# Performance work log

Hardware: AMD Instinct MI355X
Metric: run time of the kernel (lower is better)

The kernel has to match this reference:

```python
import jax, jax.numpy as jnp
import numpy as np

EMB = 64          # emb_size
LG = 64           # lg_msg_dim
NDB = 16          # num_dist_basis
NCB = 16          # num_cos_basis
NCLS = 40
NLAYERS = 2
NJK = NLAYERS + 2  # jumping-knowledge sequence length
HID = (NJK * EMB) // 2  # PyG JK-LSTM hidden size = 128


def setup_inputs() -> dict:
    key = jax.random.key(0)
    ks = jax.random.split(key, 24)
    N, Eg, Elg, F = 50000, 800000, 800000, 128
    s = 0.05
    inp = {
        "x": jax.random.normal(ks[0], (N, F), jnp.float32),
        "edge_index_g": jax.random.randint(ks[1], (2, Eg), 0, N, jnp.int32),
        "edge_attr_g": jax.random.uniform(ks[2], (Eg, NDB), jnp.float32),
        "edge_index_lg": jax.random.randint(ks[3], (2, Elg), 0, Eg, jnp.int32),
        "edge_attr_lg": jax.random.uniform(ks[4], (Elg, NCB), jnp.float32),
        # parameters (nn.Linear convention: W is [out, in])
        "W_feat": jax.random.normal(ks[5], (EMB, F), jnp.float32) * s,
        "W_msg": jax.random.normal(ks[6], (LG, 2 * EMB + NDB), jnp.float32) * s,
        "W_lg2g": jax.random.normal(ks[7], (EMB, LG), jnp.float32) * s,
        "b_lg2g": jax.random.normal(ks[8], (EMB,), jnp.float32) * s,
        "W_msg_layers": jax.random.normal(ks[9], (NLAYERS, LG, 2 * LG + NCB), jnp.float32) * s,
        # bidirectional LSTM params (PyTorch gate order i,f,g,o)
        "Wih_f": jax.random.normal(ks[10], (4 * HID, EMB), jnp.float32) * s,
        "Whh_f": jax.random.normal(ks[11], (4 * HID, HID), jnp.float32) * s,
        "bih_f": jax.random.normal(ks[12], (4 * HID,), jnp.float32) * s,
        "bhh_f": jax.random.normal(ks[13], (4 * HID,), jnp.float32) * s,
        "Wih_b": jax.random.normal(ks[14], (4 * HID, EMB), jnp.float32) * s,
        "Whh_b": jax.random.normal(ks[15], (4 * HID, HID), jnp.float32) * s,
        "bih_b": jax.random.normal(ks[16], (4 * HID,), jnp.float32) * s,
        "bhh_b": jax.random.normal(ks[17], (4 * HID,), jnp.float32) * s,
        "W_att": jax.random.normal(ks[18], (1, 2 * HID), jnp.float32) * s,
        "b_att": jax.random.normal(ks[19], (1,), jnp.float32) * s,
        "W_out": jax.random.normal(ks[20], (NCLS, EMB), jnp.float32) * s,
    }
    return inp


def _lstm(x_seq, Wih, Whh, bih, bhh, reverse):
    # x_seq: [N, L, C] -> hs: [N, L, H]
    N = x_seq.shape[0]
    H = Whh.shape[1]
    b = bih + bhh

    def step(carry, x_t):
        h, c = carry
        gates = x_t @ Wih.T + h @ Whh.T + b
        i, f, g, o = jnp.split(gates, 4, axis=-1)
        c = jax.nn.sigmoid(f) * c + jax.nn.sigmoid(i) * jnp.tanh(g)
        h = jax.nn.sigmoid(o) * jnp.tanh(c)
        return (h, c), h

    xs = jnp.swapaxes(x_seq, 0, 1)  # [L, N, C]
    init = (jnp.zeros((N, H), x_seq.dtype), jnp.zeros((N, H), x_seq.dtype))
    _, hs = jax.lax.scan(step, init, xs, reverse=reverse)
    return jnp.swapaxes(hs, 0, 1)


def reference(x, edge_index_g, edge_attr_g, edge_index_lg, edge_attr_lg,
              W_feat, W_msg, W_lg2g, b_lg2g, W_msg_layers,
              Wih_f, Whh_f, bih_f, bhh_f, Wih_b, Whh_b, bih_b, bhh_b,
              W_att, b_att, W_out):
    N = x.shape[0]
    Eg = edge_attr_g.shape[0]
    seg = jax.ops.segment_sum

    # node embedding (eval mode: dropout is identity)
    node_emb = jax.nn.relu(x @ W_feat.T)  # [N, EMB]

    # initial linegraph node features: gather endpoints -> concat -> linear -> relu
    m1 = node_emb[edge_index_g[0]]  # [Eg, EMB]
    m2 = node_emb[edge_index_g[1]]
    msg_emb = jax.nn.relu(jnp.concatenate([m1, m2, edge_attr_g], -1) @ W_msg.T)  # [Eg, LG]

    node_embs = [node_emb]
    msg_red = msg_emb @ W_lg2g.T + b_lg2g
    node_embs.append(seg(msg_red, edge_index_g[1], num_segments=N))

    # message-passing layers on the linegraph
    for l in range(W_msg_layers.shape[0]):
        s = msg_emb[edge_index_lg[0]]
        d = msg_emb[edge_index_lg[1]]
        m = jax.nn.relu(jnp.concatenate([s, d, edge_attr_lg], -1) @ W_msg_layers[l].T)
        msg_emb = seg(m, edge_index_lg[1], num_segments=Eg)  # scatter_add over linegraph
        incoming = seg(msg_emb, edge_index_g[1], num_segments=N)
        node_embs.append(incoming @ W_lg2g.T + b_lg2g)

    # JumpingKnowledge ('lstm'): bidirectional LSTM -> attention -> weighted sum
    x_jk = jnp.stack(node_embs, axis=1)  # [N, NJK, EMB]
    h_f = _lstm(x_jk, Wih_f, Whh_f, bih_f, bhh_f, reverse=False)
    h_b = _lstm(x_jk, Wih_b, Whh_b, bih_b, bhh_b, reverse=True)
    h = jnp.concatenate([h_f, h_b], -1)  # [N, NJK, 2*HID]
    alpha = jax.nn.softmax((h @ W_att.T + b_att)[..., 0], axis=-1)  # [N, NJK]
    final_emb = jnp.sum(x_jk * alpha[..., None], axis=1)  # [N, EMB]

    out = final_emb @ W_out.T
    return jax.nn.log_softmax(out, axis=-1)
```

## Files before the change

### kernel.cpp

```cpp
#include <hip/hip_runtime.h>

typedef unsigned short u16;
typedef unsigned int u32;
typedef __attribute__((ext_vector_type(8))) short bf16x8;
typedef __attribute__((ext_vector_type(4))) float f32x4;

#define MFMA(a, b, c) __builtin_amdgcn_mfma_f32_16x16x32_bf16(a, b, c, 0, 0, 0)

__device__ __forceinline__ u16 f2bf(float x) {
    union { float f; u32 u; } v; v.f = x;
    u32 r = (v.u + 0x7FFFu + ((v.u >> 16) & 1u)) >> 16;
    return (u16)r;
}
__device__ __forceinline__ float bf2f(u16 b) {
    union { u32 u; float f; } v; v.u = ((u32)b) << 16;
    return v.f;
}
__device__ __forceinline__ void casAddPair(u32* w, float lo, float hi) {
    u32 old = *w, assumed;
    do {
        assumed = old;
        u32 des = (u32)f2bf(bf2f((u16)(assumed & 0xFFFFu)) + lo) |
                  ((u32)f2bf(bf2f((u16)(assumed >> 16)) + hi) << 16);
        if (des == assumed) break;
        old = atomicCAS(w, assumed, des);
    } while (old != assumed);
}

__global__ __launch_bounds__(256) void prep_w(
    const float* __restrict__ Whh_f, const float* __restrict__ Whh_b,
    const float* __restrict__ Wih_f, const float* __restrict__ Wih_b,
    const float* __restrict__ bih_f, const float* __restrict__ bhh_f,
    const float* __restrict__ bih_b, const float* __restrict__ bhh_b,
    const float* __restrict__ W_feat, const float* __restrict__ W_msg,
    const float* __restrict__ W_msg_l, const float* __restrict__ W_lg2g,
    u16* __restrict__ WhhB, u16* __restrict__ WihB, float* __restrict__ BS,
    u16* __restrict__ WfeatB, u16* __restrict__ WmsgB,
    u16* __restrict__ WmsgLB, u16* __restrict__ Wlg2gB)
{
    const float L2E = 1.4426950408889634f;
    int i = blockIdx.x * 256 + threadIdx.x;
    if (i < 131072) {
        int d = i >> 16, r = i & 65535;
        float s = (((r >> 14) & 3) == 2) ? 2.f * L2E : L2E;
        WhhB[i] = f2bf(s * (d ? Whh_b[r] : Whh_f[r]));
    } else if (i < 196608) {
        int i2 = i - 131072; int d = i2 >> 15, r = i2 & 32767;
        float s = (((r >> 13) & 3) == 2) ? 2.f * L2E : L2E;
        WihB[i2] = f2bf(s * (d ? Wih_b[r] : Wih_f[r]));
    } else if (i < 197632) {
        int i3 = i - 196608; int d = i3 >> 9, g = i3 & 511;
        float s = (((g >> 7) & 3) == 2) ? 2.f * L2E : L2E;
        BS[i3] = s * (d ? (bih_b[g] + bhh_b[g]) : (bih_f[g] + bhh_f[g]));
    } else if (i < 205824) {
        int j = i - 197632; WfeatB[j] = f2bf(W_feat[j]);
    } else if (i < 215040) {
        int j = i - 205824; WmsgB[j] = f2bf(W_msg[j]);
    } else if (i < 233472) {
        int j = i - 215040; WmsgLB[j] = f2bf(W_msg_l[j]);
    } else if (i < 237568) {
        int j = i - 233472; Wlg2gB[j] = f2bf(W_lg2g[j]);
    }
}

__global__ __launch_bounds__(256) void count_kernel(const int* __restrict__ dst,
                                                    u32* __restrict__ cnt, long E)
{
    long i = (long)blockIdx.x * 256 + threadIdx.x;
    if (i < E) atomicAdd(&cnt[dst[i]], 1u);
}

__global__ __launch_bounds__(256) void scan1(const u32* __restrict__ a,
                                             u32* __restrict__ part, int n)
{
    __shared__ u32 ts[256];
    int b = blockIdx.x, t = threadIdx.x;
    long i0 = (long)b * 1024 + t * 4;
    u32 s = 0;
#pragma unroll
    for (int k = 0; k < 4; ++k) { long i = i0 + k; if (i < n) s += a[i]; }
    ts[t] = s; __syncthreads();
    for (int off = 1; off < 256; off <<= 1) {
        u32 x = (t >= off) ? ts[t - off] : 0u;
        __syncthreads(); ts[t] += x; __syncthreads();
    }
    if (t == 255) part[b] = ts[255];
}

__global__ __launch_bounds__(1024) void scan2(u32* __restrict__ part, int nb,
                                              u32* __restrict__ total_out)
{
    __shared__ u32 ts[1024];
    int t = threadIdx.x;
    u32 v = (t < nb) ? part[t] : 0u;
    ts[t] = v; __syncthreads();
    for (int off = 1; off < 1024; off <<= 1) {
        u32 x = (t >= off) ? ts[t - off] : 0u;
        __syncthreads(); ts[t] += x; __syncthreads();
    }
    if (t < nb) part[t] = ts[t] - v;
    if (t == 1023 && total_out) *total_out = ts[1023];
}

__global__ __launch_bounds__(256) void scan3(u32* __restrict__ a,
                                             const u32* __restrict__ part, int n)
{
    __shared__ u32 ts[256];
    int b = blockIdx.x, t = threadIdx.x;
    long i0 = (long)b * 1024 + t * 4;
    u32 v[4]; u32 s = 0;
#pragma unroll
    for (int k = 0; k < 4; ++k) { long i = i0 + k; v[k] = (i < n) ? a[i] : 0u; s += v[k]; }
    ts[t] = s; __syncthreads();
    for (int off = 1; off < 256; off <<= 1) {
        u32 x = (t >= off) ? ts[t - off] : 0u;
        __syncthreads(); ts[t] += x; __syncthreads();
    }
    u32 run = part[b] + ts[t] - s;
#pragma unroll
    for (int k = 0; k < 4; ++k) {
        long i = i0 + k;
        if (i < n) { u32 x = v[k]; a[i] = run; run += x; }
    }
}

__global__ __launch_bounds__(256) void fill_kernel(const int* __restrict__ dst,
                                                   u32* __restrict__ off,
                                                   int* __restrict__ list, long E)
{
    long i = (long)blockIdx.x * 256 + threadIdx.x;
    if (i < E) {
        u32 pos = atomicAdd(&off[dst[i]], 1u);
        list[pos] = (int)i;
    }
}

__global__ __launch_bounds__(256) void zero_fill(const u32* __restrict__ offc,
                                                 u16* __restrict__ outb, long NB)
{
    long idx = (long)blockIdx.x * 256 + threadIdx.x;
    long n = idx >> 3; int q = (int)(idx & 7);
    if (n >= NB) return;
    u32 s = n ? offc[n - 1] : 0u;
    u32 e = offc[n];
    bool need = (s == e) || ((s >> 7) != ((e - 1) >> 7));
    if (need) *(uint4*)(outb + n * 64 + q * 8) = make_uint4(0, 0, 0, 0);
}

template <int K, bool RELU, bool INBF16>
__global__ __launch_bounds__(256) void rowgemm(
    const void* __restrict__ in, const u16* __restrict__ W,
    const float* __restrict__ bias, const float* __restrict__ bias_scale,
    u16* __restrict__ outb, int M)
{
    constexpr int KP = K + 8;
    constexpr int K8 = K / 8;
    __shared__ u16 inS[64 * KP];
    __shared__ u16 WS[64 * KP];
    int t = threadIdx.x;
    long rb = (long)blockIdx.x * 64;
    for (int i = t; i < 64 * K8; i += 256) {
        int c = i / K8, q = i - c * K8;
        *(uint4*)&WS[c * KP + q * 8] = *(const uint4*)&W[c * K + q * 8];
    }
    if (INBF16) {
        const u16* inb = (const u16*)in;
        for (int i = t; i < 64 * K8; i += 256) {
            int r = i / K8, q = i - r * K8;
            long gr = rb + r;
            uint4 v = make_uint4(0, 0, 0, 0);
            if (gr < M) v = *(const uint4*)&inb[gr * (long)K + q * 8];
            *(uint4*)&inS[r * KP + q * 8] = v;
        }
    } else {
        const float* inf = (const float*)in;
        for (int i = t; i < 64 * K; i += 256) {
            int r = i / K, k = i - r * K;
            long gr = rb + r;
            inS[r * KP + k] = (gr < M) ? f2bf(inf[gr * (long)K + k]) : (u16)0;
        }
    }
    __syncthreads();
    int l = t & 63, w = t >> 6, lr = l & 15, lq = l >> 4;
    f32x4 acc[4];
#pragma unroll
    for (int i = 0; i < 4; ++i) acc[i] = (f32x4){0.f, 0.f, 0.f, 0.f};
#pragma unroll
    for (int kc = 0; kc < K; kc += 32) {
        bf16x8 a = *(const bf16x8*)&inS[(w * 16 + lr) * KP + kc + lq * 8];
#pragma unroll
        for (int ct = 0; ct < 4; ++ct) {
            bf16x8 b = *(const bf16x8*)&WS[(ct * 16 + lr) * KP + kc + lq * 8];
            acc[ct] = MFMA(a, b, acc[ct]);
        }
    }
#pragma unroll
    for (int ct = 0; ct < 4; ++ct)
#pragma unroll
        for (int r = 0; r < 4; ++r) {
            long gr = rb + w * 16 + lq * 4 + r;
            if (gr < M) {
                int c = ct * 16 + lr;
                float v = acc[ct][r];
                if (bias) v += bias[c] * (bias_scale ? bias_scale[gr] : 1.f);
                if (RELU) v = fmaxf(v, 0.f);
                outb[gr * 64 + c] = f2bf(v);
            }
        }
}

__global__ __launch_bounds__(512, 4) void edge_msg_init2(
    const u16* __restrict__ feat, const int* __restrict__ ei,
    const float* __restrict__ attr, const u16* __restrict__ W,
    u16* __restrict__ outb, long E)
{
    __shared__ u16 WS[64 * 168];
    __shared__ u16 eds[128 * 64];
    int t = threadIdx.x;
    long eb = (long)blockIdx.x * 128;
    for (int i = t; i < 1152; i += 512) {
        int c = i / 18, q = i - c * 18;
        *(uint4*)&WS[c * 168 + q * 8] = *(const uint4*)&W[c * 144 + q * 8];
    }
    if (t < 192) {
        int c = t / 3, q = t - c * 3;
        *(uint4*)&WS[c * 168 + 144 + q * 8] = make_uint4(0, 0, 0, 0);
    }
    int w = t >> 6, l = t & 63, lr = l & 15, lq = l >> 4;
    long e = eb + w * 16 + lr;
    long ec = (e < E) ? e : (E - 1);
    int src = ei[ec], dst = ei[E + ec];
    bf16x8 A[5];
    {
        const uint4* sp = (const uint4*)(feat + (long)src * 64);
        const uint4* dp = (const uint4*)(feat + (long)dst * 64);
        *(uint4*)&A[0] = sp[lq];
        *(uint4*)&A[1] = sp[4 + lq];
        *(uint4*)&A[2] = dp[lq];
        *(uint4*)&A[3] = dp[4 + lq];
        uint4 pv = make_uint4(0, 0, 0, 0);
        if (lq < 2) {
            const float4* ap = (const float4*)(attr + ec * 16) + lq * 2;
            float4 b0 = ap[0], b1 = ap[1];
            pv.x = (u32)f2bf(b0.x) | ((u32)f2bf(b0.y) << 16);
            pv.y = (u32)f2bf(b0.z) | ((u32)f2bf(b0.w) << 16);
            pv.z = (u32)f2bf(b1.x) | ((u32)f2bf(b1.y) << 16);
            pv.w = (u32)f2bf(b1.z) | ((u32)f2bf(b1.w) << 16);
        }
        *(uint4*)&A[4] = pv;
    }
    __syncthreads();
    f32x4 acc[4];
#pragma unroll
    for (int ct = 0; ct < 4; ++ct) acc[ct] = (f32x4){0.f, 0.f, 0.f, 0.f};
#pragma unroll
    for (int kc = 0; kc < 5; ++kc) {
#pragma unroll
        for (int ct = 0; ct < 4; ++ct) {
            bf16x8 b = *(const bf16x8*)&WS[(ct * 16 + lr) * 168 + kc * 32 + lq * 8];
            acc[ct] = MFMA(A[kc], b, acc[ct]);
        }
    }
#pragma unroll
    for (int ct = 0; ct < 4; ++ct)
#pragma unroll
        for (int r = 0; r < 4; ++r) {
            int row = w * 16 + lq * 4 + r;
            int col = ct * 16 + lr;
            eds[row * 64 + col] = f2bf(fmaxf(acc[ct][r], 0.f));
        }
    __syncthreads();
    for (int j = t; j < 1024; j += 512) {
        int le = j >> 3, q = j & 7;
        long e2 = eb + le;
        if (e2 < E)
            *(uint4*)(outb + e2 * 64 + q * 8) = *(const uint4*)&eds[le * 64 + q * 8];
    }
}

__global__ __launch_bounds__(512, 4) void edge_msg_lg2(
    const u16* __restrict__ feat, const int* __restrict__ ei,
    const float* __restrict__ attr, const u16* __restrict__ W,
    const int* __restrict__ list, u16* __restrict__ outb, long E)
{
    __shared__ u16 WS[64 * 168];
    __shared__ u16 eds[128 * 64];
    __shared__ int dstS[128];
    __shared__ int idS[128];
    __shared__ int srcS[128];
    __shared__ int dprevS, dnextS;
    int t = threadIdx.x;
    long pb = (long)blockIdx.x * 128;
    for (int i = t; i < 1152; i += 512) {
        int c = i / 18, q = i - c * 18;
        *(uint4*)&WS[c * 168 + q * 8] = *(const uint4*)&W[c * 144 + q * 8];
    }
    if (t < 192) {
        int c = t / 3, q = t - c * 3;
        *(uint4*)&WS[c * 168 + 144 + q * 8] = make_uint4(0, 0, 0, 0);
    }
    if (t < 128) {
        long p = pb + t;
        int id = (p < E) ? list[p] : -1;
        idS[t] = id;
        srcS[t] = (id >= 0) ? ei[id] : 0;
        dstS[t] = (id >= 0) ? ei[E + id] : -1;
    } else if (t == 128) {
        dprevS = (pb > 0) ? ei[E + list[pb - 1]] : -2;
    } else if (t == 129) {
        dnextS = (pb + 128 < E) ? ei[E + list[pb + 128]] : -2;
    }
    __syncthreads();
    int w = t >> 6, l = t & 63, lr = l & 15, lq = l >> 4;
    int el = w * 16 + lr;
    int id = idS[el];
    long idc = (id >= 0) ? (long)id : 0;
    int src = srcS[el];
    int dst = (dstS[el] >= 0) ? dstS[el] : 0;
    bf16x8 A[5];
    {
        const uint4* sp = (const uint4*)(feat + (long)src * 64);
        const uint4* dp = (const uint4*)(feat + (long)dst * 64);
        *(uint4*)&A[0] = sp[lq];
        *(uint4*)&A[1] = sp[4 + lq];
        *(uint4*)&A[2] = dp[lq];
        *(uint4*)&A[3] = dp[4 + lq];
        uint4 pv = make_uint4(0, 0, 0, 0);
        if (lq < 2) {
            const float4* ap = (const float4*)(attr + idc * 16) + lq * 2;
            float4 b0 = ap[0], b1 = ap[1];
            pv.x = (u32)f2bf(b0.x) | ((u32)f2bf(b0.y) << 16);
            pv.y = (u32)f2bf(b0.z) | ((u32)f2bf(b0.w) << 16);
            pv.z = (u32)f2bf(b1.x) | ((u32)f2bf(b1.y) << 16);
            pv.w = (u32)f2bf(b1.z) | ((u32)f2bf(b1.w) << 16);
        }
        *(uint4*)&A[4] = pv;
    }
    f32x4 acc[4];
#pragma unroll
    for (int ct = 0; ct < 4; ++ct) acc[ct] = (f32x4){0.f, 0.f, 0.f, 0.f};
#pragma unroll
    for (int kc = 0; kc < 5; ++kc) {
#pragma unroll
        for (int ct = 0; ct < 4; ++ct) {
            bf16x8 b = *(const bf16x8*)&WS[(ct * 16 + lr) * 168 + kc * 32 + lq * 8];
            acc[ct] = MFMA(A[kc], b, acc[ct]);
        }
    }
#pragma unroll
    for (int ct = 0; ct < 4; ++ct)
#pragma unroll
        for (int r = 0; r < 4; ++r) {
            int row = w * 16 + lq * 4 + r;
            int col = ct * 16 + lr;
            eds[row * 64 + col] = f2bf(fmaxf(acc[ct][r], 0.f));
        }
    __syncthreads();
    for (int j = t; j < 4096; j += 512) {
        int le = j >> 5, wd = j & 31;
        int d = dstS[le];
        if (d < 0) continue;
        if (le > 0 && dstS[le - 1] == d) continue;
        float lo = 0.f, hi = 0.f;
        int le2 = le;
        do {
            u32 pair = *(const u32*)&eds[le2 * 64 + wd * 2];
            lo += bf2f((u16)(pair & 0xFFFFu));
            hi += bf2f((u16)(pair >> 16));
            ++le2;
        } while (le2 < 128 && dstS[le2] == d);
        bool bprev = (le == 0 && dprevS == d);
        bool bnext = (le2 == 128 && dnextS == d);
        u32* dw = (u32*)(outb + (long)d * 64 + wd * 2);
        if (bprev || bnext) {
            casAddPair(dw, lo, hi);
        } else {
            *dw = (u32)f2bf(lo) | ((u32)f2bf(hi) << 16);
        }
    }
}

__global__ __launch_bounds__(256) void gather_g(
    const u16* __restrict__ m, const int* __restrict__ list,
    const u32* __restrict__ offc, u16* __restrict__ aggB,
    float* __restrict__ degOut, int N)
{
    int t = threadIdx.x;
    int wv = t >> 6, c = t & 31, half = (t >> 5) & 1;
    long n = (long)blockIdx.x * 4 + wv;
    if (n >= N) return;
    u32 start = n ? offc[n - 1] : 0u;
    u32 end = offc[n];
    float s0 = 0.f, s1 = 0.f;
    for (u32 i = start + half; i < end; i += 2) {
        int e = list[i];
        u32 pair = *(const u32*)&m[(long)e * 64 + c * 2];
        s0 += bf2f((u16)(pair & 0xFFFFu));
        s1 += bf2f((u16)(pair >> 16));
    }
    s0 += __shfl_xor(s0, 32);
    s1 += __shfl_xor(s1, 32);
    if (half == 0)
        *(u32*)&aggB[n * 64 + c * 2] = (u32)f2bf(s0) | ((u32)f2bf(s1) << 16);
    if (degOut && c == 0 && half == 0) degOut[n] = (float)(end - start);
}

__global__ __launch_bounds__(512, 2) void lstm3(
    const u16* __restrict__ jkB, const u16* __restrict__ WhhB,
    const u16* __restrict__ WihB, const float* __restrict__ BS,
    const float* __restrict__ Watt, float* __restrict__ scores,
    int N)
{
    __shared__ u16 hS[64 * 136];
    __shared__ u16 xS[4][64 * 72];
    __shared__ float bsS[512];
    __shared__ float part[4 * 64 * 8];
    int t = threadIdx.x;
    int dir = blockIdx.y;
    int w = t >> 6, l = t & 63, lr = l & 15, lq = l >> 4;
    const u16* WhhD = WhhB + (long)dir * 65536;
    const u16* WihD = WihB + (long)dir * 32768;
    long n0 = (long)blockIdx.x * 64;

    {
        int n = t >> 3, j = t & 7;
        long gn = n0 + n;
#pragma unroll
        for (int k = 0; k < 4; ++k) {
            uint4 v = make_uint4(0, 0, 0, 0);
            if (gn < N) v = *(const uint4*)&jkB[((long)k * N + gn) * 64 + j * 8];
            *(uint4*)&xS[k][n * 72 + j * 8] = v;
        }
    }
    bsS[t] = BS[dir * 512 + t];

    int grow0 = w * 16 + lq * 4;
    bf16x8 Wh[4][4];
#pragma unroll
    for (int ty = 0; ty < 4; ++ty) {
        int g = ty * 128 + w * 16 + lr;
#pragma unroll
        for (int kc = 0; kc < 4; ++kc)
            Wh[ty][kc] = *(const bf16x8*)&WhhD[g * 128 + kc * 32 + lq * 8];
    }
    const u16* pWiBase = WihD + (w * 16 + lr) * 64 + lq * 8;
    float4 Wa4 = *(const float4*)&Watt[dir * 128 + grow0];
    float* scOut = scores + (long)dir * N * 4;

    float creg[4][4] = {};
    __syncthreads();

#pragma unroll 1
    for (int s = 0; s < 4; ++s) {
        int tt = dir ? (3 - s) : s;
        const u16* pW = pWiBase;
        asm volatile("" : "+v"(pW));
        float u[4][4];
        {
            bf16x8 wi0 = *(const bf16x8*)(pW);
            bf16x8 wi1 = *(const bf16x8*)(pW + 32);
            bf16x8 wg0 = *(const bf16x8*)(pW + 16384);
            bf16x8 wg1 = *(const bf16x8*)(pW + 16416);
            f32x4 bi = *(const f32x4*)&bsS[grow0];
            f32x4 bg = *(const f32x4*)&bsS[256 + grow0];
            f32x4 acc[2][4];
#pragma unroll
            for (int nt = 0; nt < 4; ++nt) { acc[0][nt] = bi; acc[1][nt] = bg; }
            if (s) {
#pragma unroll
                for (int kc = 0; kc < 4; ++kc) {
                    bf16x8 a[4];
#pragma unroll
                    for (int nt = 0; nt < 4; ++nt)
                        a[nt] = *(const bf16x8*)&hS[(nt * 16 + lr) * 136 + kc * 32 + lq * 8];
#pragma unroll
                    for (int nt = 0; nt < 4; ++nt) {
                        acc[0][nt] = MFMA(Wh[0][kc], a[nt], acc[0][nt]);
                        acc[1][nt] = MFMA(Wh[2][kc], a[nt], acc[1][nt]);
                    }
                }
            }
#pragma unroll
            for (int kc = 0; kc < 2; ++kc) {
                bf16x8 wi = kc ? wi1 : wi0;
                bf16x8 wg = kc ? wg1 : wg0;
                bf16x8 a[4];
#pragma unroll
                for (int nt = 0; nt < 4; ++nt)
                    a[nt] = *(const bf16x8*)&xS[tt][(nt * 16 + lr) * 72 + kc * 32 + lq * 8];
#pragma unroll
                for (int nt = 0; nt < 4; ++nt) {
                    acc[0][nt] = MFMA(wi, a[nt], acc[0][nt]);
                    acc[1][nt] = MFMA(wg, a[nt], acc[1][nt]);
                }
            }
#pragma unroll
            for (int nt = 0; nt < 4; ++nt)
#pragma unroll
                for (int r = 0; r < 4; ++r) {
                    float si = __builtin_amdgcn_rcpf(
                        1.f + __builtin_amdgcn_exp2f(-acc[0][nt][r]));
                    float tg = 2.f * __builtin_amdgcn_rcpf(
                        1.f + __builtin_amdgcn_exp2f(-acc[1][nt][r])) - 1.f;
                    u[nt][r] = si * tg;
                }
        }
        {
            bf16x8 wf0 = *(const bf16x8*)(pW + 8192);
            bf16x8 wf1 = *(const bf16x8*)(pW + 8224);
            bf16x8 wo0 = *(const bf16x8*)(pW + 24576);
            bf16x8 wo1 = *(const bf16x8*)(pW + 24608);
            f32x4 bfv = *(const f32x4*)&bsS[128 + grow0];
            f32x4 bov = *(const f32x4*)&bsS[384 + grow0];
            f32x4 acc[2][4];
#pragma unroll
            for (int nt = 0; nt < 4; ++nt) { acc[0][nt] = bfv; acc[1][nt] = bov; }
            if (s) {
#pragma unroll
                for (int kc = 0; kc < 4; ++kc) {
                    bf16x8 a[4];
#pragma unroll
                    for (int nt = 0; nt < 4; ++nt)
                        a[nt] = *(const bf16x8*)&hS[(nt * 16 + lr) * 136 + kc * 32 + lq * 8];
#pragma unroll
                    for (int nt = 0; nt < 4; ++nt) {
                        acc[0][nt] = MFMA(Wh[1][kc], a[nt], acc[0][nt]);
                        acc[1][nt] = MFMA(Wh[3][kc], a[nt], acc[1][nt]);
                    }
                }
            }
#pragma unroll
            for (int kc = 0; kc < 2; ++kc) {
                bf16x8 wf = kc ? wf1 : wf0;
                bf16x8 wo = kc ? wo1 : wo0;
                bf16x8 a[4];
#pragma unroll
                for (int nt = 0; nt < 4; ++nt)
                    a[nt] = *(const bf16x8*)&xS[tt][(nt * 16 + lr) * 72 + kc * 32 + lq * 8];
#pragma unroll
                for (int nt = 0; nt < 4; ++nt) {
                    acc[0][nt] = MFMA(wf, a[nt], acc[0][nt]);
                    acc[1][nt] = MFMA(wo, a[nt], acc[1][nt]);
                }
            }
            if (s) __syncthreads();
#pragma unroll
            for (int nt = 0; nt < 4; ++nt) {
                float hv[4];
#pragma unroll
                for (int r = 0; r < 4; ++r) {
                    float sf = __builtin_amdgcn_rcpf(
                        1.f + __builtin_amdgcn_exp2f(-acc[0][nt][r]));
                    float c = sf * creg[nt][r] + u[nt][r];
                    float so = __builtin_amdgcn_rcpf(
                        1.f + __builtin_amdgcn_exp2f(-acc[1][nt][r]));
                    float th = 2.f * __builtin_amdgcn_rcpf(
                        1.f + __builtin_amdgcn_exp2f(-2.8853900817779268f * c)) - 1.f;
                    creg[nt][r] = c;
                    hv[r] = so * th;
                }
                float p = hv[0] * Wa4.x + hv[1] * Wa4.y + hv[2] * Wa4.z + hv[3] * Wa4.w;
                p += __shfl_xor(p, 16);
                p += __shfl_xor(p, 32);
                if (lq == 0) part[(tt * 64 + nt * 16 + lr) * 8 + w] = p;
                if (s < 3) {
                    u32 p0, p1;
                    asm("v_cvt_pk_bf16_f32 %0, %1, %2" : "=v"(p0) : "v"(hv[0]), "v"(hv[1]));
                    asm("v_cvt_pk_bf16_f32 %0, %1, %2" : "=v"(p1) : "v"(hv[2]), "v"(hv[3]));
                    *(uint2*)&hS[(nt * 16 + lr) * 136 + grow0] = make_uint2(p0, p1);
                }
            }
        }
        if (s < 3) __syncthreads();
    }
    __syncthreads();
    if (t < 256) {
        int tt = t >> 6, node = t & 63;
        long gn = n0 + node;
        if (gn < N) {
            const float4* pp = (const float4*)&part[(tt * 64 + node) * 8];
            float4 a = pp[0], b = pp[1];
            scOut[gn * 4 + tt] = a.x + a.y + a.z + a.w + b.x + b.y + b.z + b.w;
        }
    }
}

__global__ __launch_bounds__(256) void final_kernel(
    const u16* __restrict__ jkB, const float* __restrict__ scores,
    const float* __restrict__ Wout, float* __restrict__ out, int N)
{
    __shared__ float feS[4][64];
    int t = threadIdx.x, l = t & 63, w = t >> 6;
    long n = (long)blockIdx.x * 4 + w;
    bool ok = (n < N);
    long nn = ok ? n : (long)(N - 1);
    float sc[4];
#pragma unroll
    for (int tt = 0; tt < 4; ++tt)
        sc[tt] = scores[nn * 4 + tt] + scores[(long)N * 4 + nn * 4 + tt];
    float m = fmaxf(fmaxf(sc[0], sc[1]), fmaxf(sc[2], sc[3]));
    float e0 = __expf(sc[0] - m), e1 = __expf(sc[1] - m);
    float e2 = __expf(sc[2] - m), e3 = __expf(sc[3] - m);
    float den = e0 + e1 + e2 + e3;
    float a0 = e0 / den, a1 = e1 / den, a2 = e2 / den, a3 = e3 / den;
    float fe = a0 * bf2f(jkB[nn * 64 + l]) + a1 * bf2f(jkB[((long)N + nn) * 64 + l]) +
               a2 * bf2f(jkB[((long)2 * N + nn) * 64 + l]) +
               a3 * bf2f(jkB[((long)3 * N + nn) * 64 + l]);
    feS[w][l] = fe;
    __syncthreads();
    float logit = 0.f;
    if (l < 40)
        for (int c = 0; c < 64; ++c) logit += feS[w][c] * Wout[l * 64 + c];
    float v = (l < 40) ? logit : -1e30f;
    for (int off = 32; off; off >>= 1) v = fmaxf(v, __shfl_xor(v, off));
    float ex = (l < 40) ? __expf(logit - v) : 0.f;
    for (int off = 32; off; off >>= 1) ex += __shfl_xor(ex, off);
    if (ok && l < 40) out[n * 40 + l] = logit - v - __logf(ex);
}

extern "C" void kernel_launch(void* const* d_in, const int* in_sizes, int n_in,
                              void* d_out, int out_size, void* d_ws, size_t ws_size,
                              hipStream_t stream)
{
    const float* x        = (const float*)d_in[0];
    const int*   eig      = (const int*)d_in[1];
    const float* eag      = (const float*)d_in[2];
    const int*   eilg     = (const int*)d_in[3];
    const float* ealg     = (const float*)d_in[4];
    const float* W_feat   = (const float*)d_in[5];
    const float* W_msg    = (const float*)d_in[6];
    const float* W_lg2g   = (const float*)d_in[7];
    const float* b_lg2g   = (const float*)d_in[8];
    const float* W_msg_l  = (const float*)d_in[9];
    const float* Wih_f    = (const float*)d_in[10];
    const float* Whh_f    = (const float*)d_in[11];
    const float* bih_f    = (const float*)d_in[12];
    const float* bhh_f    = (const float*)d_in[13];
    const float* Wih_b    = (const float*)d_in[14];
    const float* Whh_b    = (const float*)d_in[15];
    const float* bih_b    = (const float*)d_in[16];
    const float* bhh_b    = (const float*)d_in[17];
    const float* W_att    = (const float*)d_in[18];
    const float* W_out    = (const float*)d_in[20];

    int  N   = in_sizes[0] / 128;
    long Eg  = in_sizes[1] / 2;
    long Elg = in_sizes[3] / 2;

    char* wp = (char*)d_ws;
    auto alloc = [&](size_t bytes) -> char* {
        char* p = wp; wp += (bytes + 255) & ~(size_t)255; return p;
    };
    u16*   jkB    = (u16*)  alloc((size_t)4 * N * 64 * 2);
    u16*   mA     = (u16*)  alloc((size_t)Eg * 64 * 2);
    u16*   mB     = (u16*)  alloc((size_t)Eg * 64 * 2);
    u16*   aggB   = (u16*)  alloc((size_t)N * 64 * 2);
    float* deg    = (float*)alloc((size_t)N * 4);
    float* scores = (float*)alloc((size_t)2 * N * 4 * 4);
    u16*   WhhB   = (u16*)  alloc((size_t)2 * 65536 * 2);
    u16*   WihB   = (u16*)  alloc((size_t)2 * 32768 * 2);
    float* BS     = (float*)alloc((size_t)2 * 512 * 4);
    u16*   WfeatB = (u16*)  alloc((size_t)8192 * 2);
    u16*   WmsgB  = (u16*)  alloc((size_t)9216 * 2);
    u16*   WmsgLB = (u16*)  alloc((size_t)18432 * 2);
    u16*   Wlg2gB = (u16*)  alloc((size_t)4096 * 2);
    u32*   off_g  = (u32*)  alloc((size_t)(N + 1) * 4);
    int*   list_g = (int*)  alloc((size_t)Eg * 4);
    u32*   off_lg = (u32*)  alloc((size_t)(Eg + 1) * 4);
    int*   list_lg= (int*)  alloc((size_t)Elg * 4);
    u32*   part   = (u32*)  alloc((size_t)1024 * 4);

    prep_w<<<928, 256, 0, stream>>>(Whh_f, Whh_b, Wih_f, Wih_b,
                                    bih_f, bhh_f, bih_b, bhh_b,
                                    W_feat, W_msg, W_msg_l, W_lg2g,
                                    WhhB, WihB, BS,
                                    WfeatB, WmsgB, WmsgLB, Wlg2gB);
    hipMemsetAsync(off_g, 0, (size_t)(N + 1) * 4, stream);
    count_kernel<<<(int)((Eg + 255) / 256), 256, 0, stream>>>(eig + Eg, off_g, Eg);
    {
        int nb = (N + 1023) / 1024;
        scan1<<<nb, 256, 0, stream>>>(off_g, part, N);
        scan2<<<1, 1024, 0, stream>>>(part, nb, off_g + N);
        scan3<<<nb, 256, 0, stream>>>(off_g, part, N);
    }
    fill_kernel<<<(int)((Eg + 255) / 256), 256, 0, stream>>>(eig + Eg, off_g, list_g, Eg);
    hipMemsetAsync(off_lg, 0, (size_t)(Eg + 1) * 4, stream);
    count_kernel<<<(int)((Elg + 255) / 256), 256, 0, stream>>>(eilg + Elg, off_lg, Elg);
    {
        int nb = (int)((Eg + 1023) / 1024);
        scan1<<<nb, 256, 0, stream>>>(off_lg, part, (int)Eg);
        scan2<<<1, 1024, 0, stream>>>(part, nb, off_lg + Eg);
        scan3<<<nb, 256, 0, stream>>>(off_lg, part, (int)Eg);
    }
    fill_kernel<<<(int)((Elg + 255) / 256), 256, 0, stream>>>(eilg + Elg, off_lg, list_lg, Elg);

    rowgemm<128, true, false><<<(N + 63) / 64, 256, 0, stream>>>(
        x, WfeatB, nullptr, nullptr, jkB, N);
    edge_msg_init2<<<(int)((Eg + 127) / 128), 512, 0, stream>>>(
        jkB, eig, eag, WmsgB, mA, Eg);
    gather_g<<<(N + 3) / 4, 256, 0, stream>>>(mA, list_g, off_g, aggB, deg, N);
    rowgemm<64, false, true><<<(N + 63) / 64, 256, 0, stream>>>(
        aggB, Wlg2gB, b_lg2g, deg, jkB + (size_t)N * 64, N);
    zero_fill<<<(int)((Eg * 8 + 255) / 256), 256, 0, stream>>>(off_lg, mB, Eg);
    edge_msg_lg2<<<(int)((Elg + 127) / 128), 512, 0, stream>>>(
        mA, eilg, ealg, WmsgLB, list_lg, mB, Elg);
    gather_g<<<(N + 3) / 4, 256, 0, stream>>>(mB, list_g, off_g, aggB, nullptr, N);
    rowgemm<64, false, true><<<(N + 63) / 64, 256, 0, stream>>>(
        aggB, Wlg2gB, b_lg2g, nullptr, jkB + (size_t)2 * N * 64, N);
    zero_fill<<<(int)((Eg * 8 + 255) / 256), 256, 0, stream>>>(off_lg, mA, Eg);
    edge_msg_lg2<<<(int)((Elg + 127) / 128), 512, 0, stream>>>(
        mB, eilg, ealg, WmsgLB + 9216, list_lg, mA, Elg);
    gather_g<<<(N + 3) / 4, 256, 0, stream>>>(mA, list_g, off_g, aggB, nullptr, N);
    rowgemm<64, false, true><<<(N + 63) / 64, 256, 0, stream>>>(
        aggB, Wlg2gB, b_lg2g, nullptr, jkB + (size_t)3 * N * 64, N);
    {
        int ntiles = (N + 63) / 64;
        lstm3<<<dim3(ntiles, 2), 512, 0, stream>>>(
            jkB, WhhB, WihB, BS, W_att, scores, N);
    }
    final_kernel<<<(N + 3) / 4, 256, 0, stream>>>(
        jkB, scores, W_out, (float*)d_out, N);
}
```

Before: 1.044 ms.

## Fuse node gather with lg2g projection; double-buffer LSTM input staging

```diff
diff --git a/kernel.cpp b/kernel.cpp
--- a/kernel.cpp
+++ b/kernel.cpp
@@ -380,17 +380,25 @@
     }
 }
 
-__global__ __launch_bounds__(256) void gather_g(
+__global__ __launch_bounds__(256) void gather_gw(
     const u16* __restrict__ m, const int* __restrict__ list,
-    const u32* __restrict__ offc, u16* __restrict__ aggB,
-    float* __restrict__ degOut, int N)
-{
+    const u32* __restrict__ offc, const u16* __restrict__ Wg,
+    const float* __restrict__ bias, int useDeg,
+    u16* __restrict__ outb, int N)
+{
+    __shared__ u16 WS[64 * 66];
+    __shared__ float aggS[4][64];
+    __shared__ float degS[4];
     int t = threadIdx.x;
-    int wv = t >> 6, c = t & 31, half = (t >> 5) & 1;
+    for (int i = t; i < 4096; i += 256) {
+        int r = i >> 6, k = i & 63;
+        WS[k * 66 + r] = Wg[i];
+    }
+    int wv = t >> 6, l = t & 63, c = l & 31, half = l >> 5;
     long n = (long)blockIdx.x * 4 + wv;
-    if (n >= N) return;
-    u32 start = n ? offc[n - 1] : 0u;
-    u32 end = offc[n];
+    long nn = (n < N) ? n : (long)(N - 1);
+    u32 start = nn ? offc[nn - 1] : 0u;
+    u32 end = offc[nn];
     float s0 = 0.f, s1 = 0.f;
     for (u32 i = start + half; i < end; i += 2) {
         int e = list[i];
@@ -400,9 +408,16 @@
     }
     s0 += __shfl_xor(s0, 32);
     s1 += __shfl_xor(s1, 32);
-    if (half == 0)
-        *(u32*)&aggB[n * 64 + c * 2] = (u32)f2bf(s0) | ((u32)f2bf(s1) << 16);
-    if (degOut && c == 0 && half == 0) degOut[n] = (float)(end - start);
+    if (half == 0) { aggS[wv][c * 2] = s0; aggS[wv][c * 2 + 1] = s1; }
+    if (l == 0) degS[wv] = (float)(end - start);
+    __syncthreads();
+    float acc = 0.f;
+#pragma unroll 8
+    for (int k = 0; k < 64; ++k)
+        acc += aggS[wv][k] * bf2f(WS[k * 66 + l]);
+    float scale = useDeg ? degS[wv] : 1.f;
+    acc += bias[l] * scale;
+    if (n < N) outb[n * 64 + l] = f2bf(acc);
 }
 
 __global__ __launch_bounds__(512, 2) void lstm3(
@@ -412,7 +427,7 @@
     int N)
 {
     __shared__ u16 hS[64 * 136];
-    __shared__ u16 xS[4][64 * 72];
+    __shared__ u16 xS[2][64 * 72];
     __shared__ float bsS[512];
     __shared__ float part[4 * 64 * 8];
     int t = threadIdx.x;
@@ -421,16 +436,14 @@
     const u16* WhhD = WhhB + (long)dir * 65536;
     const u16* WihD = WihB + (long)dir * 32768;
     long n0 = (long)blockIdx.x * 64;
+    int pn = t >> 3, pj = t & 7;
+    long pgn = n0 + pn;
 
     {
-        int n = t >> 3, j = t & 7;
-        long gn = n0 + n;
-#pragma unroll
-        for (int k = 0; k < 4; ++k) {
-            uint4 v = make_uint4(0, 0, 0, 0);
-            if (gn < N) v = *(const uint4*)&jkB[((long)k * N + gn) * 64 + j * 8];
-            *(uint4*)&xS[k][n * 72 + j * 8] = v;
-        }
+        int tt0 = dir ? 3 : 0;
+        uint4 v = make_uint4(0, 0, 0, 0);
+        if (pgn < N) v = *(const uint4*)&jkB[((long)tt0 * N + pgn) * 64 + pj * 8];
+        *(uint4*)&xS[0][pn * 72 + pj * 8] = v;
     }
     bsS[t] = BS[dir * 512 + t];
 
@@ -453,6 +466,13 @@
 #pragma unroll 1
     for (int s = 0; s < 4; ++s) {
         int tt = dir ? (3 - s) : s;
+        int cur = s & 1;
+        uint4 xpre;
+        if (s < 3) {
+            int ttn = dir ? (2 - s) : (s + 1);
+            xpre = make_uint4(0, 0, 0, 0);
+            if (pgn < N) xpre = *(const uint4*)&jkB[((long)ttn * N + pgn) * 64 + pj * 8];
+        }
         const u16* pW = pWiBase;
         asm volatile("" : "+v"(pW));
         float u[4][4];
@@ -487,7 +507,7 @@
                 bf16x8 a[4];
 #pragma unroll
                 for (int nt = 0; nt < 4; ++nt)
-                    a[nt] = *(const bf16x8*)&xS[tt][(nt * 16 + lr) * 72 + kc * 32 + lq * 8];
+                    a[nt] = *(const bf16x8*)&xS[cur][(nt * 16 + lr) * 72 + kc * 32 + lq * 8];
 #pragma unroll
                 for (int nt = 0; nt < 4; ++nt) {
                     acc[0][nt] = MFMA(wi, a[nt], acc[0][nt]);
@@ -536,7 +556,7 @@
                 bf16x8 a[4];
 #pragma unroll
                 for (int nt = 0; nt < 4; ++nt)
-                    a[nt] = *(const bf16x8*)&xS[tt][(nt * 16 + lr) * 72 + kc * 32 + lq * 8];
+                    a[nt] = *(const bf16x8*)&xS[cur][(nt * 16 + lr) * 72 + kc * 32 + lq * 8];
 #pragma unroll
                 for (int nt = 0; nt < 4; ++nt) {
                     acc[0][nt] = MFMA(wf, a[nt], acc[0][nt]);
@@ -571,7 +591,10 @@
                 }
             }
         }
-        if (s < 3) __syncthreads();
+        if (s < 3) {
+            *(uint4*)&xS[cur ^ 1][pn * 72 + pj * 8] = xpre;
+            __syncthreads();
+        }
     }
     __syncthreads();
     if (t < 256) {
@@ -654,8 +677,6 @@
     u16*   jkB    = (u16*)  alloc((size_t)4 * N * 64 * 2);
     u16*   mA     = (u16*)  alloc((size_t)Eg * 64 * 2);
     u16*   mB     = (u16*)  alloc((size_t)Eg * 64 * 2);
-    u16*   aggB   = (u16*)  alloc((size_t)N * 64 * 2);
-    float* deg    = (float*)alloc((size_t)N * 4);
     float* scores = (float*)alloc((size_t)2 * N * 4 * 4);
     u16*   WhhB   = (u16*)  alloc((size_t)2 * 65536 * 2);
     u16*   WihB   = (u16*)  alloc((size_t)2 * 32768 * 2);
@@ -698,21 +719,18 @@
         x, WfeatB, nullptr, nullptr, jkB, N);
     edge_msg_init2<<<(int)((Eg + 127) / 128), 512, 0, stream>>>(
         jkB, eig, eag, WmsgB, mA, Eg);
-    gather_g<<<(N + 3) / 4, 256, 0, stream>>>(mA, list_g, off_g, aggB, deg, N);
-    rowgemm<64, false, true><<<(N + 63) / 64, 256, 0, stream>>>(
-        aggB, Wlg2gB, b_lg2g, deg, jkB + (size_t)N * 64, N);
+    gather_gw<<<(N + 3) / 4, 256, 0, stream>>>(
+        mA, list_g, off_g, Wlg2gB, b_lg2g, 1, jkB + (size_t)N * 64, N);
     zero_fill<<<(int)((Eg * 8 + 255) / 256), 256, 0, stream>>>(off_lg, mB, Eg);
     edge_msg_lg2<<<(int)((Elg + 127) / 128), 512, 0, stream>>>(
         mA, eilg, ealg, WmsgLB, list_lg, mB, Elg);
-    gather_g<<<(N + 3) / 4, 256, 0, stream>>>(mB, list_g, off_g, aggB, nullptr, N);
-    rowgemm<64, false, true><<<(N + 63) / 64, 256, 0, stream>>>(
-        aggB, Wlg2gB, b_lg2g, nullptr, jkB + (size_t)2 * N * 64, N);
+    gather_gw<<<(N + 3) / 4, 256, 0, stream>>>(
+        mB, list_g, off_g, Wlg2gB, b_lg2g, 0, jkB + (size_t)2 * N * 64, N);
     zero_fill<<<(int)((Eg * 8 + 255) / 256), 256, 0, stream>>>(off_lg, mA, Eg);
     edge_msg_lg2<<<(int)((Elg + 127) / 128), 512, 0, stream>>>(
         mB, eilg, ealg, WmsgLB + 9216, list_lg, mA, Elg);
-    gather_g<<<(N + 3) / 4, 256, 0, stream>>>(mA, list_g, off_g, aggB, nullptr, N);
-    rowgemm<64, false, true><<<(N + 63) / 64, 256, 0, stream>>>(
-        aggB, Wlg2gB, b_lg2g, nullptr, jkB + (size_t)3 * N * 64, N);
+    gather_gw<<<(N + 3) / 4, 256, 0, stream>>>(
+        mA, list_g, off_g, Wlg2gB, b_lg2g, 0, jkB + (size_t)3 * N * 64, N);
     {
         int ntiles = (N + 63) / 64;
         lstm3<<<dim3(ntiles, 2), 512, 0, stream>>>(
```

Result: slower. 1.065 ms (+2.0%).
